# Optimization experiments

Hardware: AMD Instinct MI355X
Metric: run time of the kernel (lower is better)

The kernel has to match this reference:

```python
import jax, jax.numpy as jnp
import numpy as np

C_IN = 64
C_H = 128
K = 5  # filter_size
EPS = 1e-5


def _conv1x1(w, x):
    # w: [O, I], x: [B, I, H, W]
    return jnp.einsum('oi,bihw->bohw', w, x)


def _conv3x3(w, x):
    # w: [O, I, 3, 3], x: [B, I, H, W], SAME padding
    return jax.lax.conv_general_dilated(
        x, w, window_strides=(1, 1), padding='SAME',
        dimension_numbers=('NCHW', 'OIHW', 'NCHW'))


def _layernorm_c(x, g, b):
    # LayerNorm over the channel dim (original permutes to NHWC, norms last dim)
    m = jnp.mean(x, axis=1, keepdims=True)
    v = jnp.mean(jnp.square(x - m), axis=1, keepdims=True)
    xn = (x - m) * jax.lax.rsqrt(v + EPS)
    return xn * g[None, :, None, None] + b[None, :, None, None]


def _dynamic_filter(x, w_df1, w_df2):
    # 3x3 conv -> ReLU -> 1x1 conv producing C_H*K*K channels
    h = jax.nn.relu(_conv3x3(w_df1, x))
    return _conv1x1(w_df2, h)


def _apply_dynamic_filter(feat, filt):
    # feat: [B, C, H, W]; filt: [B, C*K*K, H, W]
    # Equivalent to unfold(K, pad=K//2) * filt summed over the K*K taps,
    # but computed as K*K shifted multiply-accumulates (no huge intermediate).
    B, C, H, W = feat.shape
    filt = filt.reshape(B, C, K * K, H, W)
    p = K // 2
    fp = jnp.pad(feat, ((0, 0), (0, 0), (p, p), (p, p)))
    out = jnp.zeros_like(feat)
    k = 0
    for ki in range(K):
        for kj in range(K):
            out = out + fp[:, :, ki:ki + H, kj:kj + W] * filt[:, :, k]
            k += 1
    return out


def setup_inputs() -> dict:
    key = jax.random.key(0)
    ks = jax.random.split(key, 8)
    B, H, W = 2, 128, 128
    s = 0.05
    return {
        'rgb_high': jax.random.normal(ks[0], (B, C_IN, H, W), jnp.float32),
        'event': jax.random.normal(ks[1], (B, C_IN, H, W), jnp.float32),
        'w_in': jax.random.normal(ks[2], (C_H, C_IN), jnp.float32) * s,
        'ln_g': jnp.ones((C_H,), jnp.float32),
        'ln_b': jnp.zeros((C_H,), jnp.float32),
        'w_df1': jax.random.normal(ks[3], (C_H, C_H, 3, 3), jnp.float32) * s,
        'w_df2': jax.random.normal(ks[4], (C_H * K * K, C_H), jnp.float32) * s,
        'w_sp': jax.random.normal(ks[5], (C_H, C_H), jnp.float32) * s,
        'w_out': jax.random.normal(ks[6], (C_IN, C_H), jnp.float32) * s,
    }


def reference(rgb_high, event, w_in, ln_g, ln_b, w_df1, w_df2, w_sp, w_out):
    rgb_feat = _layernorm_c(_conv1x1(w_in, rgb_high), ln_g, ln_b)
    event_feat = _layernorm_c(_conv1x1(w_in, event), ln_g, ln_b)
    rgb_filter = _dynamic_filter(rgb_feat, w_df1, w_df2)
    event_filter = _dynamic_filter(event_feat, w_df1, w_df2)
    rgb_enh = _apply_dynamic_filter(rgb_feat, rgb_filter)
    event_enh = _apply_dynamic_filter(event_feat, event_filter)
    rgb_filtered = rgb_enh * jax.nn.sigmoid(_conv1x1(w_sp, event_enh))
    rgb_fused = rgb_enh + rgb_filtered + rgb_feat
    rgb_norm = _layernorm_c(rgb_fused, ln_g, ln_b)
    return _conv1x1(w_out, rgb_norm)
```

## Files before the change

kernel.cpp:

```cpp
#include <hip/hip_runtime.h>
#include <math.h>

#define BLK 256

typedef unsigned short ushort;
typedef unsigned int uint;
typedef __attribute__((ext_vector_type(8))) short short8;
typedef __attribute__((ext_vector_type(4))) float f32x4;

constexpr int C_Hc = 128;
constexpr int C_INc = 64;
constexpr int Hh = 128;
constexpr int Ww = 128;
constexpr int HWc = Hh * Ww;
constexpr int Bb = 2;
constexpr float EPSV = 1e-5f;

__device__ __forceinline__ float bf2f(ushort u) {
    union { uint u32; float f; } v; v.u32 = (uint)u << 16; return v.f;
}
__device__ __forceinline__ ushort f2bf(float x) {
    union { float f; uint u; } v; v.f = x;
    uint r = (v.u + 0x7FFFu + ((v.u >> 16) & 1u)) >> 16;
    return (ushort)r;
}
__device__ __forceinline__ uint pack2(float a, float b) {
    return (uint)f2bf(a) | ((uint)f2bf(b) << 16);
}
__device__ __forceinline__ void gload16(const ushort* g, ushort* l) {
    __builtin_amdgcn_global_load_lds(
        (const __attribute__((address_space(1))) void*)g,
        (__attribute__((address_space(3))) void*)l, 16, 0, 0);
}

__global__ __launch_bounds__(BLK) void k_prep(
    const float* __restrict__ w1, const float* __restrict__ w2,
    const float* __restrict__ wsp,
    ushort* __restrict__ wA, ushort* __restrict__ w2b,
    ushort* __restrict__ wspb)
{
    int idx = blockIdx.x * BLK + threadIdx.x;
    if (idx < 147456) {
        int tap = idx >> 14, r = idx & 16383;
        int chunk = r >> 10, co = (r >> 3) & 127, e = r & 7;
        int ci = chunk * 8 + e;
        wA[idx] = f2bf(w1[(co * 128 + ci) * 9 + tap]);
    } else if (idx < 557056) {
        int o = idx - 147456;
        int k = o >> 14, r = o & 16383;
        int chunk = r >> 10, co = (r >> 3) & 127, e = r & 7;
        int ci = chunk * 8 + e;
        w2b[o] = f2bf(w2[(co * 25 + k) * 128 + ci]);
    } else if (idx < 573440) {
        int o = idx - 557056;
        int chunk = o >> 10, co = (o >> 3) & 127, e = o & 7;
        wspb[o] = f2bf(wsp[co * 128 + chunk * 8 + e]);
    }
}

__global__ __launch_bounds__(BLK) void k_in_ln(
    const float* __restrict__ xr, const float* __restrict__ xe,
    const float* __restrict__ w_in, const float* __restrict__ lng,
    const float* __restrict__ lnb,
    ushort* __restrict__ fTr, ushort* __restrict__ fTe,
    float* __restrict__ featrT)
{
    int bid  = blockIdx.x;
    int simg = bid >> 9;
    int rem  = bid & 511;
    int b    = rem >> 8;
    int base = (rem & 255) * 64;
    const float* x = simg ? xe : xr;
    ushort* fT = simg ? fTe : fTr;
    int tid  = threadIdx.x;
    int lane = tid & 63;
    int cg   = tid >> 6;

    __shared__ float xs[C_INc][64];
    __shared__ float r1[4][64], r2[4][64];
    __shared__ ushort lb[64][136];
    __shared__ float  lf[64][132];

    #pragma unroll
    for (int r = 0; r < 16; ++r) {
        int i = cg * 16 + r;
        xs[i][lane] = x[(b * C_INc + i) * HWc + base + lane];
    }
    __syncthreads();

    float acc[32];
    #pragma unroll
    for (int cc = 0; cc < 32; ++cc) acc[cc] = 0.f;

    for (int i4 = 0; i4 < 16; ++i4) {
        float x0 = xs[i4 * 4 + 0][lane];
        float x1 = xs[i4 * 4 + 1][lane];
        float x2 = xs[i4 * 4 + 2][lane];
        float x3 = xs[i4 * 4 + 3][lane];
        #pragma unroll
        for (int cc = 0; cc < 32; ++cc) {
            float4 wv = *reinterpret_cast<const float4*>(
                &w_in[(cg * 32 + cc) * C_INc + i4 * 4]);
            acc[cc] += wv.x * x0 + wv.y * x1 + wv.z * x2 + wv.w * x3;
        }
    }

    float s1 = 0.f, s2 = 0.f;
    #pragma unroll
    for (int cc = 0; cc < 32; ++cc) { s1 += acc[cc]; s2 += acc[cc] * acc[cc]; }
    r1[cg][lane] = s1; r2[cg][lane] = s2;
    __syncthreads();
    float m   = (r1[0][lane] + r1[1][lane] + r1[2][lane] + r1[3][lane]) * (1.f / C_Hc);
    float ex2 = (r2[0][lane] + r2[1][lane] + r2[2][lane] + r2[3][lane]) * (1.f / C_Hc);
    float rs  = rsqrtf(ex2 - m * m + EPSV);

    #pragma unroll
    for (int cc = 0; cc < 32; cc += 4) {
        int c0 = cg * 32 + cc;
        float4 g4 = *reinterpret_cast<const float4*>(&lng[c0]);
        float4 b4 = *reinterpret_cast<const float4*>(&lnb[c0]);
        float4 y;
        y.x = (acc[cc + 0] - m) * rs * g4.x + b4.x;
        y.y = (acc[cc + 1] - m) * rs * g4.y + b4.y;
        y.z = (acc[cc + 2] - m) * rs * g4.z + b4.z;
        y.w = (acc[cc + 3] - m) * rs * g4.w + b4.w;
        *reinterpret_cast<uint*>(&lb[lane][c0])     = pack2(y.x, y.y);
        *reinterpret_cast<uint*>(&lb[lane][c0 + 2]) = pack2(y.z, y.w);
        if (!simg)
            *reinterpret_cast<float4*>(&lf[lane][c0]) = y;
    }
    __syncthreads();

    long long tb = ((long long)((b << 14) + base)) << 7;
    #pragma unroll
    for (int t = 0; t < 4; ++t) {
        int j  = tid + (t << 8);
        int px = j >> 4;
        int w0 = (j & 15) << 3;
        uint4 v = *reinterpret_cast<const uint4*>(&lb[px][w0]);
        *reinterpret_cast<uint4*>(&fT[tb + ((long long)px << 7) + w0]) = v;
    }
    if (!simg) {
        #pragma unroll
        for (int t = 0; t < 8; ++t) {
            int j  = tid + (t << 8);
            int px = j >> 5;
            int w0 = (j & 31) << 2;
            float4 v = *reinterpret_cast<const float4*>(&lf[px][w0]);
            *reinterpret_cast<float4*>(&featrT[tb + ((long long)px << 7) + w0]) = v;
        }
    }
}

__global__ __launch_bounds__(512, 2) void k_conv3(
    const ushort* __restrict__ fTr, const ushort* __restrict__ fTe,
    const ushort* __restrict__ wA,
    ushort* __restrict__ hTr, ushort* __restrict__ hTe)
{
    int bid = blockIdx.x;
    int s = bid >> 8, b = (bid >> 7) & 1, h0 = bid & 127;
    const ushort* fT = s ? fTe : fTr;
    ushort* hT = s ? hTe : hTr;
    int tid = threadIdx.x, lane = tid & 63, wv = tid >> 6;
    int lpx = lane & 15, lk = lane >> 4;
    int co0 = (wv & 3) * 32, px0 = (wv >> 2) * 64;

    __shared__ ushort ft[16 * 390 * 8];
    __shared__ ushort wk[16 * 128 * 8];

    const long long ibase = (long long)(b << 14);

    for (int i = tid; i < 6240; i += 512) {
        int chunk = i / 390;
        int rem = i - chunk * 390;
        int row = rem / 130, col = rem - row * 130;
        int gh = h0 + row - 1, gw = col - 1;
        uint4 v = make_uint4(0, 0, 0, 0);
        if ((unsigned)gh < 128u && (unsigned)gw < 128u)
            v = *reinterpret_cast<const uint4*>(
                &fT[((ibase + (gh << 7) + gw) << 7) + (chunk << 3)]);
        *reinterpret_cast<uint4*>(&ft[i << 3]) = v;
    }

    uint4 wpre[4];
    #pragma unroll
    for (int t = 0; t < 4; ++t)
        wpre[t] = *reinterpret_cast<const uint4*>(&wA[(tid + (t << 9)) << 3]);
    __syncthreads();
    #pragma unroll
    for (int t = 0; t < 4; ++t)
        *reinterpret_cast<uint4*>(&wk[(tid + (t << 9)) << 3]) = wpre[t];
    __syncthreads();

    f32x4 acc[2][4];
    #pragma unroll
    for (int f = 0; f < 2; ++f)
        #pragma unroll
        for (int p = 0; p < 4; ++p) acc[f][p] = f32x4{0.f, 0.f, 0.f, 0.f};

    for (int tap = 0; tap < 9; ++tap) {
        int ki = tap / 3, kj = tap - ki * 3;
        if (tap < 8) {
            const ushort* srcb = &wA[(tap + 1) << 14];
            #pragma unroll
            for (int t = 0; t < 4; ++t)
                wpre[t] = *reinterpret_cast<const uint4*>(
                    &srcb[(tid + (t << 9)) << 3]);
        }
        short8 a[2][4];
        #pragma unroll
        for (int f = 0; f < 2; ++f) {
            int co = co0 + f * 16 + lpx;
            #pragma unroll
            for (int q = 0; q < 4; ++q)
                a[f][q] = *reinterpret_cast<const short8*>(
                    &wk[(((q * 4 + lk) << 7) + co) << 3]);
        }
        #pragma unroll
        for (int p = 0; p < 4; ++p) {
            int col = px0 + p * 16 + lpx + kj;
            short8 bq[4];
            #pragma unroll
            for (int q = 0; q < 4; ++q)
                bq[q] = *reinterpret_cast<const short8*>(
                    &ft[((q * 4 + lk) * 390 + ki * 130 + col) << 3]);
            #pragma unroll
            for (int f = 0; f < 2; ++f)
                #pragma unroll
                for (int q = 0; q < 4; ++q)
                    acc[f][p] = __builtin_amdgcn_mfma_f32_16x16x32_bf16(
                        a[f][q], bq[q], acc[f][p], 0, 0, 0);
        }
        __syncthreads();
        if (tap < 8) {
            #pragma unroll
            for (int t = 0; t < 4; ++t)
                *reinterpret_cast<uint4*>(&wk[(tid + (t << 9)) << 3]) = wpre[t];
        }
        __syncthreads();
    }

    long long obase = (ibase + ((long long)h0 << 7)) << 7;
    #pragma unroll
    for (int f = 0; f < 2; ++f)
        #pragma unroll
        for (int p = 0; p < 4; ++p) {
            int c  = co0 + f * 16 + (lk << 2);
            int px = px0 + p * 16 + lpx;
            float v0 = fmaxf(acc[f][p][0], 0.f), v1 = fmaxf(acc[f][p][1], 0.f);
            float v2 = fmaxf(acc[f][p][2], 0.f), v3 = fmaxf(acc[f][p][3], 0.f);
            ushort* dst = &hT[obase + ((long long)px << 7) + c];
            *reinterpret_cast<uint*>(&dst[0]) = pack2(v0, v1);
            *reinterpret_cast<uint*>(&dst[2]) = pack2(v2, v3);
        }
}

__global__ __launch_bounds__(512, 2) void k_dfapply(
    const ushort* __restrict__ hTr, const ushort* __restrict__ hTe,
    const ushort* __restrict__ fTr, const ushort* __restrict__ fTe,
    const ushort* __restrict__ w2b,
    ushort* __restrict__ enhr, ushort* __restrict__ enhe)
{
    int bid = blockIdx.x;
    int s = bid >> 7, b = (bid >> 6) & 1, hp = bid & 63;
    int h0g = hp << 1;
    const ushort* hT = s ? hTe : hTr;
    const ushort* fT = s ? fTe : fTr;
    ushort* enh = s ? enhe : enhr;
    int tid = threadIdx.x, lane = tid & 63, wv = tid >> 6;
    int lpx = lane & 15, lk = lane >> 4;
    int r    = wv >> 2;
    int co0  = (wv & 1) * 64, px0 = ((wv >> 1) & 1) * 64;
    int h0   = h0g + r;

    __shared__ ushort wk[2][16 * 128 * 8];
    __shared__ ushort fr[2][128 * 16 * 8];

    const long long ibase = (long long)(b << 14);
    const long long rowbase = (ibase + ((long long)h0 << 7)) << 7;

    short8 bq[4][4];
    #pragma unroll
    for (int p = 0; p < 4; ++p) {
        int px = px0 + p * 16 + lpx;
        #pragma unroll
        for (int q = 0; q < 4; ++q)
            bq[p][q] = *reinterpret_cast<const short8*>(
                &hT[rowbase + ((long long)px << 7) + ((q * 4 + lk) << 3)]);
    }

    auto stage_rows = [&](int dh) {
        for (int rr = 0; rr < 2; ++rr) {
            int gh = h0g + rr + dh;
            if ((unsigned)gh < 128u) {
                const ushort* rowsrc = fT + ((ibase + ((long long)gh << 7)) << 7);
                #pragma unroll
                for (int t = 0; t < 4; ++t) {
                    int j = tid + (t << 9);
                    int px = j >> 4, u = j & 15;
                    int su = u ^ (px & 15);
                    gload16(&rowsrc[(px << 7) + (su << 3)], &fr[rr][j << 3]);
                }
            }
        }
    };

    #pragma unroll
    for (int t = 0; t < 4; ++t) {
        int j = tid + (t << 9);
        gload16(&w2b[j << 3], &wk[0][j << 3]);
    }
    stage_rows(-2);
    __syncthreads();

    f32x4 osum[4][4];
    #pragma unroll
    for (int f = 0; f < 4; ++f)
        #pragma unroll
        for (int p = 0; p < 4; ++p) osum[f][p] = f32x4{0.f, 0.f, 0.f, 0.f};

    for (int k = 0; k < 25; ++k) {
        int cur = k & 1;
        if (k < 24) {
            const ushort* srcb = &w2b[(k + 1) << 14];
            #pragma unroll
            for (int t = 0; t < 4; ++t) {
                int j = tid + (t << 9);
                gload16(&srcb[j << 3], &wk[cur ^ 1][j << 3]);
            }
        }
        int k5 = k / 5;
        int dh = k5 - 2, dw = k - k5 * 5 - 2;
        int gh = h0 + dh;
        bool rowok = (unsigned)gh < 128u;

        uint2 featv[4][4];
        #pragma unroll
        for (int p = 0; p < 4; ++p) {
            int gw = px0 + p * 16 + lpx + dw;
            bool ok = rowok && ((unsigned)gw < 128u);
            #pragma unroll
            for (int f = 0; f < 4; ++f) {
                int c4 = co0 + f * 16 + (lk << 2);
                uint2 v = make_uint2(0, 0);
                if (ok) v = *reinterpret_cast<const uint2*>(
                    &fr[r][(((gw << 4) + ((c4 >> 3) ^ (gw & 15))) << 3)
                           + (c4 & 7)]);
                featv[p][f] = v;
            }
        }

        #pragma unroll
        for (int f = 0; f < 4; ++f) {
            int co = co0 + f * 16 + lpx;
            short8 a[4];
            #pragma unroll
            for (int q = 0; q < 4; ++q)
                a[q] = *reinterpret_cast<const short8*>(
                    &wk[cur][(((q * 4 + lk) << 7) + co) << 3]);
            __builtin_amdgcn_s_setprio(1);
            #pragma unroll
            for (int p = 0; p < 4; ++p) {
                f32x4 fac = f32x4{0.f, 0.f, 0.f, 0.f};
                #pragma unroll
                for (int q = 0; q < 4; ++q)
                    fac = __builtin_amdgcn_mfma_f32_16x16x32_bf16(
                        a[q], bq[p][q], fac, 0, 0, 0);
                uint2 fv = featv[p][f];
                osum[f][p][0] += fac[0] * bf2f((ushort)(fv.x & 0xffff));
                osum[f][p][1] += fac[1] * bf2f((ushort)(fv.x >> 16));
                osum[f][p][2] += fac[2] * bf2f((ushort)(fv.y & 0xffff));
                osum[f][p][3] += fac[3] * bf2f((ushort)(fv.y >> 16));
            }
            __builtin_amdgcn_s_setprio(0);
        }
        __syncthreads();
        if ((k % 5 == 4) && k < 24) {
            stage_rows(k / 5 - 1);
            __syncthreads();
        }
    }

    #pragma unroll
    for (int f = 0; f < 4; ++f)
        #pragma unroll
        for (int p = 0; p < 4; ++p) {
            int c  = co0 + f * 16 + (lk << 2);
            int px = px0 + p * 16 + lpx;
            int slot = (c >> 3) ^ (px & 15);
            uint2 o;
            o.x = pack2(osum[f][p][0], osum[f][p][1]);
            o.y = pack2(osum[f][p][2], osum[f][p][3]);
            *reinterpret_cast<uint2*>(
                &fr[r][(((px << 4) + slot) << 3) + (c & 7)]) = o;
        }
    __syncthreads();

    #pragma unroll
    for (int t = 0; t < 8; ++t) {
        int j  = tid + (t << 9);
        int rr = j >> 11;
        int jj = j & 2047;
        int px = jj >> 4, u = jj & 15;
        int chunk = u ^ (px & 15);
        uint4 v = *reinterpret_cast<const uint4*>(&fr[rr][jj << 3]);
        *reinterpret_cast<uint4*>(
            &enh[((ibase + ((long long)(h0g + rr) << 7)) << 7)
                 + ((long long)px << 7) + (chunk << 3)]) = v;
    }
}

__global__ __launch_bounds__(BLK, 2) void k_final(
    const ushort* __restrict__ enhr, const ushort* __restrict__ enhe,
    const float* __restrict__ featrT,
    const ushort* __restrict__ wspb, const float* __restrict__ w_out,
    const float* __restrict__ lng, const float* __restrict__ lnb,
    float* __restrict__ out)
{
    int bid = blockIdx.x;
    int b = bid >> 8;
    int px0g = (bid & 255) * 64;
    int tid = threadIdx.x, lane = tid & 63, wv = tid >> 6;
    int lpx = lane & 15, lk = lane >> 4;

    __shared__ float woA[4096];
    __shared__ float woB[4096];
    __shared__ float xs[128][64];
    __shared__ float p1[4][64], p2[4][64];
    ushort* es = (ushort*)woA;

    const long long ebase = ((long long)((b << 14) + px0g)) << 7;

    #pragma unroll
    for (int t = 0; t < 4; ++t) {
        int j = tid + (t << 8);
        int chunk = j >> 6, px = j & 63;
        *reinterpret_cast<uint4*>(&es[j << 3]) =
            *reinterpret_cast<const uint4*>(
                &enhe[ebase + ((long long)px << 7) + (chunk << 3)]);
    }
    __syncthreads();

    int co0 = wv * 32;
    f32x4 sp[2][4];
    #pragma unroll
    for (int f = 0; f < 2; ++f)
        #pragma unroll
        for (int p = 0; p < 4; ++p) sp[f][p] = f32x4{0.f, 0.f, 0.f, 0.f};
    #pragma unroll
    for (int q = 0; q < 4; ++q) {
        short8 a[2], bb[4];
        #pragma unroll
        for (int f = 0; f < 2; ++f)
            a[f] = *reinterpret_cast<const short8*>(
                &wspb[((((q * 4 + lk) << 7) + co0 + f * 16 + lpx)) << 3]);
        #pragma unroll
        for (int p = 0; p < 4; ++p)
            bb[p] = *reinterpret_cast<const short8*>(
                &es[((((q * 4 + lk) << 6) + p * 16 + lpx)) << 3]);
        #pragma unroll
        for (int f = 0; f < 2; ++f)
            #pragma unroll
            for (int p = 0; p < 4; ++p)
                sp[f][p] = __builtin_amdgcn_mfma_f32_16x16x32_bf16(
                    a[f], bb[p], sp[f][p], 0, 0, 0);
    }

    float fu[2][4][4];
    float s1[4] = {0.f, 0.f, 0.f, 0.f}, s2[4] = {0.f, 0.f, 0.f, 0.f};
    #pragma unroll
    for (int f = 0; f < 2; ++f) {
        int c4 = co0 + f * 16 + (lk << 2);
        #pragma unroll
        for (int p = 0; p < 4; ++p) {
            int px = p * 16 + lpx;
            long long poff = ebase + ((long long)px << 7) + c4;
            uint2 re2 = *reinterpret_cast<const uint2*>(&enhr[poff]);
            float4 rf4 = *reinterpret_cast<const float4*>(&featrT[poff]);
            float re[4] = { bf2f((ushort)(re2.x & 0xffff)), bf2f((ushort)(re2.x >> 16)),
                            bf2f((ushort)(re2.y & 0xffff)), bf2f((ushort)(re2.y >> 16)) };
            float rf[4] = { rf4.x, rf4.y, rf4.z, rf4.w };
            #pragma unroll
            for (int rr = 0; rr < 4; ++rr) {
                float sg = 1.f / (1.f + __expf(-sp[f][p][rr]));
                float v = re[rr] * (1.f + sg) + rf[rr];
                fu[f][p][rr] = v;
                s1[p] += v; s2[p] += v * v;
            }
        }
    }
    #pragma unroll
    for (int p = 0; p < 4; ++p) {
        s1[p] += __shfl_xor(s1[p], 16); s1[p] += __shfl_xor(s1[p], 32);
        s2[p] += __shfl_xor(s2[p], 16); s2[p] += __shfl_xor(s2[p], 32);
    }
    if (lk == 0) {
        #pragma unroll
        for (int p = 0; p < 4; ++p) {
            p1[wv][p * 16 + lpx] = s1[p];
            p2[wv][p * 16 + lpx] = s2[p];
        }
    }
    __syncthreads();

    #pragma unroll
    for (int i = 0; i < 8; ++i) {
        int fidx = tid + (i << 8);
        float4 v = *reinterpret_cast<const float4*>(&w_out[fidx << 2]);
        if (fidx < 1024) reinterpret_cast<float4*>(woA)[fidx] = v;
        else             reinterpret_cast<float4*>(woB)[fidx - 1024] = v;
    }

    float mm[4], rs[4];
    #pragma unroll
    for (int p = 0; p < 4; ++p) {
        int px = p * 16 + lpx;
        float m   = (p1[0][px] + p1[1][px] + p1[2][px] + p1[3][px]) * (1.f / 128.f);
        float ex2 = (p2[0][px] + p2[1][px] + p2[2][px] + p2[3][px]) * (1.f / 128.f);
        mm[p] = m;
        rs[p] = rsqrtf(ex2 - m * m + EPSV);
    }

    #pragma unroll
    for (int f = 0; f < 2; ++f) {
        int c4 = co0 + f * 16 + (lk << 2);
        float4 g = *reinterpret_cast<const float4*>(&lng[c4]);
        float4 bta = *reinterpret_cast<const float4*>(&lnb[c4]);
        #pragma unroll
        for (int p = 0; p < 4; ++p) {
            int px = p * 16 + lpx;
            xs[c4 + 0][px] = (fu[f][p][0] - mm[p]) * rs[p] * g.x + bta.x;
            xs[c4 + 1][px] = (fu[f][p][1] - mm[p]) * rs[p] * g.y + bta.y;
            xs[c4 + 2][px] = (fu[f][p][2] - mm[p]) * rs[p] * g.z + bta.z;
            xs[c4 + 3][px] = (fu[f][p][3] - mm[p]) * rs[p] * g.w + bta.w;
        }
    }
    __syncthreads();

    int co0o = wv * 16;
    const float* wop = (wv & 2) ? woB : woA;
    int wbase = (wv & 1) << 11;
    float oacc[16];
    #pragma unroll
    for (int oo = 0; oo < 16; ++oo) oacc[oo] = 0.f;
    for (int j4 = 0; j4 < 32; ++j4) {
        float x0 = xs[j4 * 4 + 0][lane];
        float x1 = xs[j4 * 4 + 1][lane];
        float x2 = xs[j4 * 4 + 2][lane];
        float x3 = xs[j4 * 4 + 3][lane];
        #pragma unroll
        for (int oo = 0; oo < 16; ++oo) {
            float4 wv4 = *reinterpret_cast<const float4*>(
                &wop[wbase + oo * C_Hc + j4 * 4]);
            oacc[oo] += wv4.x * x0 + wv4.y * x1 + wv4.z * x2 + wv4.w * x3;
        }
    }
    #pragma unroll
    for (int oo = 0; oo < 16; ++oo)
        out[((long long)(b * C_INc + co0o + oo) << 14) + px0g + lane] = oacc[oo];
}

extern "C" void kernel_launch(void* const* d_in, const int* in_sizes, int n_in,
                              void* d_out, int out_size, void* d_ws, size_t ws_size,
                              hipStream_t stream)
{
    const float* rgb  = (const float*)d_in[0];
    const float* evt  = (const float*)d_in[1];
    const float* w_in = (const float*)d_in[2];
    const float* lng  = (const float*)d_in[3];
    const float* lnb  = (const float*)d_in[4];
    const float* w1   = (const float*)d_in[5];
    const float* w2   = (const float*)d_in[6];
    const float* wsp  = (const float*)d_in[7];
    const float* wout = (const float*)d_in[8];
    float* out = (float*)d_out;

    float* ws = (float*)d_ws;
    ushort* fTr    = (ushort*)(ws);
    ushort* fTe    = (ushort*)(ws + 2097152);
    ushort* hTr    = (ushort*)(ws + 4194304);
    ushort* hTe    = (ushort*)(ws + 6291456);
    ushort* enhr   = (ushort*)(ws + 8388608);
    ushort* enhe   = (ushort*)(ws + 10485760);
    float*  featrT = (float*)(ws + 12582912);
    ushort* wA     = (ushort*)(ws + 16777216);
    ushort* w2b    = (ushort*)(ws + 16850944);
    ushort* wspb   = (ushort*)(ws + 17055744);

    k_prep<<<2240, BLK, 0, stream>>>(w1, w2, wsp, wA, w2b, wspb);
    k_in_ln<<<2 * Bb * 256, BLK, 0, stream>>>(rgb, evt, w_in, lng, lnb,
                                              fTr, fTe, featrT);
    k_conv3<<<512, 512, 0, stream>>>(fTr, fTe, wA, hTr, hTe);
    k_dfapply<<<256, 512, 0, stream>>>(hTr, hTe, fTr, fTe, w2b, enhr, enhe);
    k_final<<<Bb * 256, BLK, 0, stream>>>(enhr, enhe, featrT, wspb, wout,
                                          lng, lnb, out);
}
```

Before: 238.0 us.

## Split conv3 rows into half-row blocks and read weights directly from global

The 3x3 conv kernel now uses 256-thread blocks that each cover a 64-pixel half row, doubling the grid. Weight tiles are no longer staged through LDS per tap; each wave loads its A fragments directly from global memory, which removes the two barriers per tap and the weight prefetch registers. The smaller LDS footprint allows higher occupancy, at the cost of more global/L2 weight traffic and more redundant halo loading.

```diff
diff --git a/kernel.cpp b/kernel.cpp
--- a/kernel.cpp
+++ b/kernel.cpp
@@ -152,44 +152,35 @@
     }
 }
 
-__global__ __launch_bounds__(512, 2) void k_conv3(
+__global__ __launch_bounds__(BLK, 3) void k_conv3(
     const ushort* __restrict__ fTr, const ushort* __restrict__ fTe,
     const ushort* __restrict__ wA,
     ushort* __restrict__ hTr, ushort* __restrict__ hTe)
 {
     int bid = blockIdx.x;
-    int s = bid >> 8, b = (bid >> 7) & 1, h0 = bid & 127;
+    int ph = bid & 1, h0 = (bid >> 1) & 127, b = (bid >> 8) & 1, s = bid >> 9;
+    int w0 = ph << 6;
     const ushort* fT = s ? fTe : fTr;
     ushort* hT = s ? hTe : hTr;
     int tid = threadIdx.x, lane = tid & 63, wv = tid >> 6;
     int lpx = lane & 15, lk = lane >> 4;
-    int co0 = (wv & 3) * 32, px0 = (wv >> 2) * 64;
-
-    __shared__ ushort ft[16 * 390 * 8];
-    __shared__ ushort wk[16 * 128 * 8];
+    int co0 = wv * 32;
+
+    __shared__ ushort ft[16 * 198 * 8];
 
     const long long ibase = (long long)(b << 14);
 
-    for (int i = tid; i < 6240; i += 512) {
-        int chunk = i / 390;
-        int rem = i - chunk * 390;
-        int row = rem / 130, col = rem - row * 130;
-        int gh = h0 + row - 1, gw = col - 1;
+    for (int i = tid; i < 16 * 198; i += BLK) {
+        int chunk = i / 198;
+        int rem = i - chunk * 198;
+        int row = rem / 66, col = rem - row * 66;
+        int gh = h0 + row - 1, gw = w0 + col - 1;
         uint4 v = make_uint4(0, 0, 0, 0);
         if ((unsigned)gh < 128u && (unsigned)gw < 128u)
             v = *reinterpret_cast<const uint4*>(
                 &fT[((ibase + (gh << 7) + gw) << 7) + (chunk << 3)]);
         *reinterpret_cast<uint4*>(&ft[i << 3]) = v;
     }
-
-    uint4 wpre[4];
-    #pragma unroll
-    for (int t = 0; t < 4; ++t)
-        wpre[t] = *reinterpret_cast<const uint4*>(&wA[(tid + (t << 9)) << 3]);
-    __syncthreads();
-    #pragma unroll
-    for (int t = 0; t < 4; ++t)
-        *reinterpret_cast<uint4*>(&wk[(tid + (t << 9)) << 3]) = wpre[t];
     __syncthreads();
 
     f32x4 acc[2][4];
@@ -200,13 +191,7 @@
 
     for (int tap = 0; tap < 9; ++tap) {
         int ki = tap / 3, kj = tap - ki * 3;
-        if (tap < 8) {
-            const ushort* srcb = &wA[(tap + 1) << 14];
-            #pragma unroll
-            for (int t = 0; t < 4; ++t)
-                wpre[t] = *reinterpret_cast<const uint4*>(
-                    &srcb[(tid + (t << 9)) << 3]);
-        }
+        const ushort* wtp = &wA[tap << 14];
         short8 a[2][4];
         #pragma unroll
         for (int f = 0; f < 2; ++f) {
@@ -214,16 +199,16 @@
             #pragma unroll
             for (int q = 0; q < 4; ++q)
                 a[f][q] = *reinterpret_cast<const short8*>(
-                    &wk[(((q * 4 + lk) << 7) + co) << 3]);
-        }
-        #pragma unroll
-        for (int p = 0; p < 4; ++p) {
-            int col = px0 + p * 16 + lpx + kj;
+                    &wtp[(((q * 4 + lk) << 7) + co) << 3]);
+        }
+        #pragma unroll
+        for (int p = 0; p < 4; ++p) {
+            int col = p * 16 + lpx + kj;
             short8 bq[4];
             #pragma unroll
             for (int q = 0; q < 4; ++q)
                 bq[q] = *reinterpret_cast<const short8*>(
-                    &ft[((q * 4 + lk) * 390 + ki * 130 + col) << 3]);
+                    &ft[((q * 4 + lk) * 198 + ki * 66 + col) << 3]);
             #pragma unroll
             for (int f = 0; f < 2; ++f)
                 #pragma unroll
@@ -231,13 +216,6 @@
                     acc[f][p] = __builtin_amdgcn_mfma_f32_16x16x32_bf16(
                         a[f][q], bq[q], acc[f][p], 0, 0, 0);
         }
-        __syncthreads();
-        if (tap < 8) {
-            #pragma unroll
-            for (int t = 0; t < 4; ++t)
-                *reinterpret_cast<uint4*>(&wk[(tid + (t << 9)) << 3]) = wpre[t];
-        }
-        __syncthreads();
     }
 
     long long obase = (ibase + ((long long)h0 << 7)) << 7;
@@ -246,7 +224,7 @@
         #pragma unroll
         for (int p = 0; p < 4; ++p) {
             int c  = co0 + f * 16 + (lk << 2);
-            int px = px0 + p * 16 + lpx;
+            int px = w0 + p * 16 + lpx;
             float v0 = fmaxf(acc[f][p][0], 0.f), v1 = fmaxf(acc[f][p][1], 0.f);
             float v2 = fmaxf(acc[f][p][2], 0.f), v3 = fmaxf(acc[f][p][3], 0.f);
             ushort* dst = &hT[obase + ((long long)px << 7) + c];
@@ -590,7 +568,7 @@
     k_prep<<<2240, BLK, 0, stream>>>(w1, w2, wsp, wA, w2b, wspb);
     k_in_ln<<<2 * Bb * 256, BLK, 0, stream>>>(rgb, evt, w_in, lng, lnb,
                                               fTr, fTe, featrT);
-    k_conv3<<<512, 512, 0, stream>>>(fTr, fTe, wA, hTr, hTe);
+    k_conv3<<<1024, BLK, 0, stream>>>(fTr, fTe, wA, hTr, hTe);
     k_dfapply<<<256, 512, 0, stream>>>(hTr, hTe, fTr, fTe, w2b, enhr, enhe);
     k_final<<<Bb * 256, BLK, 0, stream>>>(enhr, enhe, featrT, wspb, wout,
                                           lng, lnb, out);
```

Result: faster. 200.0 us (median of 3 runs) (-16.0%).
